# Kernel tuning notes

Measured on AMD Instinct MI355X. Metric: run time of the kernel, lower is better.

## Reference

```python
import jax, jax.numpy as jnp
import numpy as np

B, L, DIN, D, H, NL, NE, TOPK, DFF, NOUT = 128, 128, 6, 256, 8, 6, 8, 2, 1024, 5
NMOE = NL // 2
DK = D // H
EPS = 1e-5


def setup_inputs() -> dict:
    key = jax.random.key(0)
    ks = iter(jax.random.split(key, 32))
    s = 0.02
    rn = lambda shape, scale=s: jax.random.normal(next(ks), shape, dtype=jnp.float32) * scale
    return {
        "x": jax.random.normal(next(ks), (B, L, DIN), dtype=jnp.float32),
        "emb_w": rn((DIN, D)), "emb_b": jnp.zeros((D,), jnp.float32),
        # wave attention layers (stacked over NL)
        "wq": rn((NL, D, D)), "wk": rn((NL, D, D)), "wv": rn((NL, D, D)), "wo": rn((NL, D, D)),
        "wfreq": rn((NL, H), 0.1), "wphase": jnp.zeros((NL, H), jnp.float32),
        # MoE layers (stacked over NMOE, experts over NE)
        "rtw": rn((NMOE, D, NE)), "rtb": jnp.zeros((NMOE, NE), jnp.float32),
        "ew1": rn((NMOE, NE, D, DFF)), "eb1": jnp.zeros((NMOE, NE, DFF), jnp.float32),
        "ew2": rn((NMOE, NE, DFF, D)), "eb2": jnp.zeros((NMOE, NE, D), jnp.float32),
        "ln_g": jnp.ones((D,), jnp.float32), "ln_b": jnp.zeros((D,), jnp.float32),
        "pred_w": rn((D, NOUT)), "pred_b": jnp.zeros((NOUT,), jnp.float32),
        "unc_w": rn((D, NOUT)), "unc_b": jnp.zeros((NOUT,), jnp.float32),
    }


def _wave_attn(x, Wq, Wk, Wv, Wo, freq, phase):
    # x: (B, L, D)
    q = (x @ Wq).reshape(B, L, H, DK).transpose(0, 2, 1, 3)  # (B,H,L,DK)
    k = (x @ Wk).reshape(B, L, H, DK).transpose(0, 2, 1, 3)
    v = (x @ Wv).reshape(B, L, H, DK).transpose(0, 2, 1, 3)
    pos = jnp.arange(L, dtype=x.dtype)
    wave = jnp.cos(2.0 * np.pi * freq[:, None] * pos[None, :] + phase[:, None])  # (H,L)
    scores = jnp.einsum("bhqd,bhkd->bhqk", q, k) * (DK ** -0.5)
    scores = scores * wave[None, :, None, :]  # modulate along key axis
    attn = jax.nn.softmax(scores, axis=-1)
    out = jnp.einsum("bhqk,bhkd->bhqd", attn, v)
    out = out.transpose(0, 2, 1, 3).reshape(B, L, D)
    return out @ Wo


def _moe(x, rw, rb, w1, b1, w2, b2):
    # x: (B, L, D). Dense per-expert compute + top-k combine weights
    xf = x.reshape(-1, D)  # (T, D), T = B*L
    T = xf.shape[0]
    p = jax.nn.softmax(xf @ rw + rb, axis=-1)           # (T, NE)
    tw, ti = jax.lax.top_k(p, TOPK)                      # (T, TOPK)
    tw = tw / tw.sum(axis=-1, keepdims=True)
    comb = jnp.zeros((T, NE), xf.dtype).at[jnp.arange(T)[:, None], ti].add(tw)  # (T, NE)
    h = jax.nn.gelu(jnp.einsum("td,edf->etf", xf, w1) + b1[:, None, :], approximate=False)
    eo = jnp.einsum("etf,efd->etd", h, w2) + b2[:, None, :]  # (NE, T, D)
    out = jnp.einsum("te,etd->td", comb, eo)
    return out.reshape(B, L, D)


def _forward(x, emb_w, emb_b, wq, wk, wv, wo, wfreq, wphase,
             rtw, rtb, ew1, eb1, ew2, eb2, ln_g, ln_b,
             pred_w, pred_b, unc_w, unc_b):
    h = x @ emb_w + emb_b
    for i in range(NL):
        h = _wave_attn(h, wq[i], wk[i], wv[i], wo[i], wfreq[i], wphase[i]) + h
        if i % 2 == 0 and i // 2 < NMOE:
            m = i // 2
            h = _moe(h, rtw[m], rtb[m], ew1[m], eb1[m], ew2[m], eb2[m]) + h
    mu = h.mean(axis=-1, keepdims=True)
    var = ((h - mu) ** 2).mean(axis=-1, keepdims=True)
    h = (h - mu) * jax.lax.rsqrt(var + EPS) * ln_g + ln_b
    latent = h[:, -1, :]  # (B, D)
    pred = latent @ pred_w + pred_b
    uncertainty = jax.nn.softplus(latent @ unc_w + unc_b)
    return pred, uncertainty


def reference(x, emb_w, emb_b, wq, wk, wv, wo, wfreq, wphase,
              rtw, rtb, ew1, eb1, ew2, eb2, ln_g, ln_b,
              pred_w, pred_b, unc_w, unc_b):
    return _forward(x, emb_w, emb_b, wq, wk, wv, wo, wfreq, wphase,
                    rtw, rtb, ew1, eb1, ew2, eb2, ln_g, ln_b,
                    pred_w, pred_b, unc_w, unc_b)
```

## Files before the change

### kernel.cpp

```cpp
#include <hip/hip_runtime.h>
#include <hip/hip_bf16.h>
#include <math.h>

#define B_    128
#define L_    128
#define DIN   6
#define D_    256
#define H_    8
#define NL_   6
#define NE_   8
#define DFF_  1024
#define NOUT_ 5
#define T_    (B_*L_)
#define DK_   32
#define NDESC_MAX 136

typedef unsigned short u16;
typedef __hip_bfloat16 bf16;
typedef __attribute__((ext_vector_type(8))) short short8;
typedef __attribute__((ext_vector_type(8))) unsigned short ushort8v;
typedef __attribute__((ext_vector_type(4))) unsigned short ushort4v;
typedef __attribute__((ext_vector_type(4))) float floatx4;

__device__ const int S_PRE[16] = {
    0, 98304, 99840, 100096, 100144, 100192, 106336, 106360,
    130936, 137080, 137336, 137592, 138872, 138877, 140157, 140162};
__device__ const int S_SRC[15] = {0,1,2,7,8,9,10,12,14,15,16,17,18,19,20};
#define NSMALL 140162

struct SrcPtrs { const void* p[21]; };

__device__ __forceinline__ float bf2f(u16 u) {
    return __uint_as_float(((unsigned)u) << 16);
}
__device__ __forceinline__ u16 f2bf(float f) {
    union { bf16 b; u16 u; } c; c.b = __float2bfloat16(f); return c.u;
}
__device__ __forceinline__ float gelu_f(float x) {
    return 0.5f * x * (1.0f + erff(x * 0.70710678118654752f));
}

__device__ __forceinline__ void gl_lds16(const u16* g, u16* l) {
    __builtin_amdgcn_global_load_lds(
        (const __attribute__((address_space(1))) unsigned int*)g,
        (__attribute__((address_space(3))) unsigned int*)l,
        16, 0, 0);
}

__global__ __launch_bounds__(256)
void conv_small_kernel(SrcPtrs P, float* __restrict__ dst)
{
    const int i = blockIdx.x * 256 + threadIdx.x;
    if (i >= NSMALL) return;
    int seg = 0;
    #pragma unroll
    for (int s = 1; s < 15; ++s) seg += (i >= S_PRE[s]) ? 1 : 0;
    const int off = i - S_PRE[seg];
    const void* src = P.p[S_SRC[seg]];
    const bool isbf = (((const u16*)P.p[15])[0] == 0x3F80);
    if (isbf) dst[i] = bf2f(((const u16*)src)[off]);
    else      dst[i] = ((const float*)src)[off];
}

template<int KD, int ND>
__global__ __launch_bounds__(256)
void transpose_tiled(const void* __restrict__ src, const u16* __restrict__ probe,
                     u16* __restrict__ dst, long dzs, int noff)
{
    const int z  = blockIdx.x;
    const int k0 = blockIdx.y * 64;
    const int n0 = blockIdx.z * 64;
    __shared__ u16 tile[64][66];
    const int tid = threadIdx.x;
    const bool isbf = (probe[0] == 0x3F80);

    if (isbf) {
        const u16* s = (const u16*)src + (size_t)z * KD * ND + (size_t)k0 * ND + n0;
        #pragma unroll
        for (int p = 0; p < 2; ++p) {
            const int c  = p * 256 + tid;
            const int kk = c >> 3, nn = (c & 7) * 8;
            *(ushort8v*)&tile[kk][nn] = *(const ushort8v*)(s + (size_t)kk * ND + nn);
        }
    } else {
        const float* s = (const float*)src + (size_t)z * KD * ND + (size_t)k0 * ND + n0;
        #pragma unroll
        for (int p = 0; p < 2; ++p) {
            const int c  = p * 256 + tid;
            const int kk = c >> 3, nn = (c & 7) * 8;
            float4 v0 = *(const float4*)(s + (size_t)kk * ND + nn);
            float4 v1 = *(const float4*)(s + (size_t)kk * ND + nn + 4);
            ushort8v t;
            t[0]=f2bf(v0.x); t[1]=f2bf(v0.y); t[2]=f2bf(v0.z); t[3]=f2bf(v0.w);
            t[4]=f2bf(v1.x); t[5]=f2bf(v1.y); t[6]=f2bf(v1.z); t[7]=f2bf(v1.w);
            *(ushort8v*)&tile[kk][nn] = t;
        }
    }
    __syncthreads();

    u16* d = dst + (size_t)z * dzs + (size_t)(n0 + noff) * KD + k0;
    #pragma unroll
    for (int p = 0; p < 2; ++p) {
        const int c  = p * 256 + tid;
        const int nn = c >> 3, kk = (c & 7) * 8;
        ushort8v t;
        #pragma unroll
        for (int j = 0; j < 8; ++j) t[j] = tile[kk + j][nn];
        *(ushort8v*)&d[(size_t)nn * KD + kk] = t;
    }
}

__global__ __launch_bounds__(256)
void embed_kernel(const float* __restrict__ x, const float* __restrict__ emb_w,
                  const float* __restrict__ emb_b, float* __restrict__ h,
                  u16* __restrict__ hb)
{
    const int idx = blockIdx.x * 256 + threadIdx.x;
    const int t = idx >> 8;
    const int d = idx & 255;
    float acc = emb_b[d];
    #pragma unroll
    for (int j = 0; j < DIN; ++j)
        acc += x[t * DIN + j] * emb_w[j * D_ + d];
    h[idx]  = acc;
    hb[idx] = f2bf(acc);
}

template<int EPI, int MODE, int NT>
__global__ __launch_bounds__(512, 4)
void mfma_gemm(const u16* __restrict__ A, int lda,
               const u16* __restrict__ Wt, long wzs, int ldwt,
               const float* __restrict__ biasb, long bzs,
               void* __restrict__ CoutV, int ldc,
               u16* __restrict__ hbout, int Mfixed,
               const int* __restrict__ cnt, const int* __restrict__ base_,
               const int* __restrict__ atok,
               const int* __restrict__ de, const int* __restrict__ dr,
               const int* __restrict__ ndesc)
{
    int M, r0, sbase = 0, e = 0;
    if constexpr (MODE == 0) {
        M  = Mfixed;
        r0 = blockIdx.x * 256;
        if (r0 >= M) return;
    } else {
        const int i = blockIdx.x;
        if (i >= *ndesc) return;
        e     = de[i];
        r0    = dr[i] * 256;
        sbase = base_[e];
        M     = cnt[e];
    }
    const u16*   W    = Wt + (size_t)e * wzs;
    const float* bias = biasb ? (biasb + (size_t)e * bzs) : nullptr;
    const int col0 = blockIdx.y * 128;

    __shared__ __attribute__((aligned(16))) u16 As[2][256 * 32];
    __shared__ __attribute__((aligned(16))) u16 Bs[2][128 * 32];
    __shared__ int stok[256];

    const int tid  = threadIdx.x;
    const int lane = tid & 63;
    const int wave = tid >> 6;
    const int wm = wave & 3, wn = wave >> 2;

    if constexpr (MODE == 1) {
        if (tid < 256) {
            int rr = r0 + tid;
            if (rr >= M) rr = M - 1;
            stok[tid] = atok[sbase + rr];
        }
        __syncthreads();
    }

    const int ss  = (lane & 3) ^ ((lane >> 3) & 3);
    const int rA0 = wave * 16 + (lane >> 2);
    const int rA1 = rA0 + 128;
    const int rB  = tid >> 2;
    long ar0, ar1;
    if constexpr (MODE == 1) {
        ar0 = stok[rA0];
        ar1 = stok[rA1];
    } else {
        int rr0 = r0 + rA0; if (rr0 >= M) rr0 = M - 1;
        int rr1 = r0 + rA1; if (rr1 >= M) rr1 = M - 1;
        ar0 = (MODE == 2) ? (long)(sbase + rr0) : (long)rr0;
        ar1 = (MODE == 2) ? (long)(sbase + rr1) : (long)rr1;
    }
    const u16* ga0 = A + ar0 * (long)lda + ss * 8;
    const u16* ga1 = A + ar1 * (long)lda + ss * 8;
    const u16* gw0 = W + (size_t)(col0 + rB) * ldwt + ss * 8;

    floatx4 acc[4][4];
    #pragma unroll
    for (int i = 0; i < 4; ++i)
        #pragma unroll
        for (int j = 0; j < 4; ++j)
            acc[i][j] = (floatx4){0.f, 0.f, 0.f, 0.f};

    const int fm = wm * 64 + (lane & 15);
    const int fn = wn * 64 + (lane & 15);
    const int ps = (lane >> 4) ^ ((lane >> 1) & 3);

    auto STAGE = [&](int b, int kt) {
        const int ko = kt * 32;
        gl_lds16(ga0 + ko, &As[b][wave * 512 + lane * 8]);
        gl_lds16(ga1 + ko, &As[b][4096 + wave * 512 + lane * 8]);
        gl_lds16(gw0 + ko, &Bs[b][wave * 512 + lane * 8]);
    };

    STAGE(0, 0);
    __syncthreads();

    int buf = 0;
    for (int t = 0; t < NT; ++t) {
        if (t + 1 < NT) STAGE(buf ^ 1, t + 1);

        short8 af[4], bfr[4];
        #pragma unroll
        for (int i = 0; i < 4; ++i)
            af[i]  = *(const short8*)&As[buf][(fm + 16 * i) * 32 + ps * 8];
        #pragma unroll
        for (int j = 0; j < 4; ++j)
            bfr[j] = *(const short8*)&Bs[buf][(fn + 16 * j) * 32 + ps * 8];
        #pragma unroll
        for (int i = 0; i < 4; ++i)
            #pragma unroll
            for (int j = 0; j < 4; ++j)
                acc[i][j] = __builtin_amdgcn_mfma_f32_16x16x32_bf16(
                    af[i], bfr[j], acc[i][j], 0, 0, 0);

        __syncthreads();
        buf ^= 1;
    }

    const int er = wm * 64 + ((lane >> 4) << 2);
    const int ec = wn * 64 + (lane & 15);
    #pragma unroll
    for (int i = 0; i < 4; ++i) {
        #pragma unroll
        for (int reg = 0; reg < 4; ++reg) {
            const int lrow = r0 + er + i * 16 + reg;
            if (lrow >= M) continue;
            const long crow = (MODE == 0) ? (long)lrow : (long)(sbase + lrow);
            #pragma unroll
            for (int j = 0; j < 4; ++j) {
                const int cj = col0 + ec + j * 16;
                const float val = acc[i][j][reg];
                if constexpr (EPI == 0) {
                    ((u16*)CoutV)[crow * ldc + cj] = f2bf(val);
                } else if constexpr (EPI == 1) {
                    const size_t idx = crow * ldc + cj;
                    const float nv = ((float*)CoutV)[idx] + val;
                    ((float*)CoutV)[idx] = nv;
                    hbout[idx] = f2bf(nv);
                } else if constexpr (EPI == 2) {
                    ((u16*)CoutV)[crow * ldc + cj] = f2bf(gelu_f(val + bias[cj]));
                } else {
                    ((float*)CoutV)[crow * ldc + cj] = val + bias[cj];
                }
            }
        }
    }
}

__global__ __launch_bounds__(256)
void attn_kernel(const u16* __restrict__ qkv, u16* __restrict__ o,
                 const float* __restrict__ wfreq, const float* __restrict__ wphase)
{
    const int bh = blockIdx.x;
    const int b  = bh >> 3;
    const int hh = bh & 7;

    __shared__ __attribute__((aligned(16))) u16 Qs[128][40];
    __shared__ __attribute__((aligned(16))) u16 Ks[128][40];
    __shared__ __attribute__((aligned(16))) u16 Vt[32][136];
    __shared__ __attribute__((aligned(16))) u16 Ps[128][136];
    __shared__ float wavec[128];

    const int tid  = threadIdx.x;
    const int lane = tid & 63;
    const int w    = tid >> 6;
    const int col16 = lane & 15;
    const int quad  = lane >> 4;

    const long qbase = (long)b * L_ * 768 + hh * DK_;

    {
        const int row = tid >> 1;
        const int hf  = (tid & 1) * 16;
        const u16* src = qkv + qbase + (long)row * 768 + hf;
        *(ushort8v*)&Qs[row][hf]     = *(const ushort8v*)(src);
        *(ushort8v*)&Qs[row][hf + 8] = *(const ushort8v*)(src + 8);
        *(ushort8v*)&Ks[row][hf]     = *(const ushort8v*)(src + 256);
        *(ushort8v*)&Ks[row][hf + 8] = *(const ushort8v*)(src + 264);
        #pragma unroll
        for (int j = 0; j < 16; ++j)
            Vt[hf + j][row] = src[512 + j];
    }
    if (tid < L_) {
        float f2 = 6.2831853071795864769f * wfreq[hh];
        wavec[tid] = cosf(f2 * (float)tid + wphase[hh]);
    }
    __syncthreads();

    const float scale = 0.17677669529663687f;
    float wv8[8];
    #pragma unroll
    for (int ni = 0; ni < 8; ++ni)
        wv8[ni] = scale * wavec[ni * 16 + col16];

    const int m0 = w * 32;
    floatx4 accs[2][8];
    {
        short8 a0 = *(const short8*)&Qs[m0 + col16][quad * 8];
        short8 a1 = *(const short8*)&Qs[m0 + 16 + col16][quad * 8];
        #pragma unroll
        for (int ni = 0; ni < 8; ++ni) {
            short8 bf = *(const short8*)&Ks[ni * 16 + col16][quad * 8];
            accs[0][ni] = __builtin_amdgcn_mfma_f32_16x16x32_bf16(
                a0, bf, (floatx4){0.f,0.f,0.f,0.f}, 0, 0, 0);
            accs[1][ni] = __builtin_amdgcn_mfma_f32_16x16x32_bf16(
                a1, bf, (floatx4){0.f,0.f,0.f,0.f}, 0, 0, 0);
        }
    }
    #pragma unroll
    for (int mi = 0; mi < 2; ++mi)
        #pragma unroll
        for (int ni = 0; ni < 8; ++ni)
            #pragma unroll
            for (int reg = 0; reg < 4; ++reg)
                accs[mi][ni][reg] *= wv8[ni];

    #pragma unroll
    for (int mi = 0; mi < 2; ++mi) {
        #pragma unroll
        for (int reg = 0; reg < 4; ++reg) {
            float rmax = -1e30f;
            #pragma unroll
            for (int ni = 0; ni < 8; ++ni)
                rmax = fmaxf(rmax, accs[mi][ni][reg]);
            #pragma unroll
            for (int off = 1; off < 16; off <<= 1)
                rmax = fmaxf(rmax, __shfl_xor(rmax, off));
            float e[8], rsum = 0.0f;
            #pragma unroll
            for (int ni = 0; ni < 8; ++ni) {
                e[ni] = expf(accs[mi][ni][reg] - rmax);
                rsum += e[ni];
            }
            #pragma unroll
            for (int off = 1; off < 16; off <<= 1)
                rsum += __shfl_xor(rsum, off);
            const float inv = 1.0f / rsum;
            const int row = m0 + mi * 16 + quad * 4 + reg;
            #pragma unroll
            for (int ni = 0; ni < 8; ++ni)
                Ps[row][ni * 16 + col16] = f2bf(e[ni] * inv);
        }
    }
    __syncthreads();

    floatx4 acco[2][2];
    #pragma unroll
    for (int mi = 0; mi < 2; ++mi)
        #pragma unroll
        for (int nj = 0; nj < 2; ++nj)
            acco[mi][nj] = (floatx4){0.f,0.f,0.f,0.f};
    #pragma unroll
    for (int kk = 0; kk < 4; ++kk) {
        short8 a0 = *(const short8*)&Ps[m0 + col16][kk * 32 + quad * 8];
        short8 a1 = *(const short8*)&Ps[m0 + 16 + col16][kk * 32 + quad * 8];
        short8 b0 = *(const short8*)&Vt[col16][kk * 32 + quad * 8];
        short8 b1 = *(const short8*)&Vt[16 + col16][kk * 32 + quad * 8];
        acco[0][0] = __builtin_amdgcn_mfma_f32_16x16x32_bf16(a0, b0, acco[0][0], 0, 0, 0);
        acco[0][1] = __builtin_amdgcn_mfma_f32_16x16x32_bf16(a0, b1, acco[0][1], 0, 0, 0);
        acco[1][0] = __builtin_amdgcn_mfma_f32_16x16x32_bf16(a1, b0, acco[1][0], 0, 0, 0);
        acco[1][1] = __builtin_amdgcn_mfma_f32_16x16x32_bf16(a1, b1, acco[1][1], 0, 0, 0);
    }

    const long obase = (long)b * L_ * D_ + hh * DK_;
    #pragma unroll
    for (int mi = 0; mi < 2; ++mi)
        #pragma unroll
        for (int reg = 0; reg < 4; ++reg) {
            const int row = m0 + mi * 16 + quad * 4 + reg;
            #pragma unroll
            for (int nj = 0; nj < 2; ++nj)
                o[obase + (long)row * D_ + nj * 16 + col16] =
                    f2bf(acco[mi][nj][reg]);
        }
}

__global__ __launch_bounds__(256)
void router_kernel(const float* __restrict__ h, const float* __restrict__ rtw,
                   const float* __restrict__ rtb, int* __restrict__ te,
                   float* __restrict__ twt)
{
    const int tid  = threadIdx.x;
    const int lane = tid & 63;
    const int wv   = tid >> 6;
    const int t    = blockIdx.x * 4 + wv;

    const float4 hv = ((const float4*)(h + (long)t * D_))[lane];
    const float4* rp = (const float4*)rtw;

    float lg[NE_];
    #pragma unroll
    for (int e = 0; e < NE_; ++e) lg[e] = 0.0f;
    #pragma unroll
    for (int i = 0; i < 4; ++i) {
        const int d = lane * 4 + i;
        const float xv = (i == 0) ? hv.x : (i == 1) ? hv.y : (i == 2) ? hv.z : hv.w;
        float4 wa = rp[d * 2 + 0];
        float4 wb = rp[d * 2 + 1];
        lg[0] = fmaf(xv, wa.x, lg[0]);
        lg[1] = fmaf(xv, wa.y, lg[1]);
        lg[2] = fmaf(xv, wa.z, lg[2]);
        lg[3] = fmaf(xv, wa.w, lg[3]);
        lg[4] = fmaf(xv, wb.x, lg[4]);
        lg[5] = fmaf(xv, wb.y, lg[5]);
        lg[6] = fmaf(xv, wb.z, lg[6]);
        lg[7] = fmaf(xv, wb.w, lg[7]);
    }
    #pragma unroll
    for (int off = 1; off < 64; off <<= 1)
        #pragma unroll
        for (int e = 0; e < NE_; ++e)
            lg[e] += __shfl_xor(lg[e], off);

    if (lane == 0) {
        #pragma unroll
        for (int e = 0; e < NE_; ++e) lg[e] += rtb[e];
        int i1 = 0; float v1 = lg[0];
        #pragma unroll
        for (int e = 1; e < NE_; ++e) { if (lg[e] > v1) { v1 = lg[e]; i1 = e; } }
        int i2 = (i1 == 0) ? 1 : 0; float v2 = lg[i2];
        #pragma unroll
        for (int e = 0; e < NE_; ++e) {
            if (e != i1 && lg[e] > v2) { v2 = lg[e]; i2 = e; }
        }
        float r   = expf(v2 - v1);
        float wa1 = 1.0f / (1.0f + r);
        te[2 * t]     = i1;
        te[2 * t + 1] = i2;
        twt[2 * t]     = wa1;
        twt[2 * t + 1] = r * wa1;
    }
}

__global__ __launch_bounds__(512)
void countscan_kernel(const int* __restrict__ te, int* __restrict__ cnt,
                      int* __restrict__ base_, int* __restrict__ cursor,
                      int* __restrict__ de, int* __restrict__ dr,
                      int* __restrict__ ndesc)
{
    const int tid = threadIdx.x;
    int c[NE_];
    #pragma unroll
    for (int e = 0; e < NE_; ++e) c[e] = 0;
    for (int i = tid; i < 2 * T_; i += 512) {
        const int e = te[i];
        #pragma unroll
        for (int ee = 0; ee < NE_; ++ee) c[ee] += (e == ee) ? 1 : 0;
    }
    #pragma unroll
    for (int off = 1; off < 64; off <<= 1)
        #pragma unroll
        for (int e = 0; e < NE_; ++e)
            c[e] += __shfl_xor(c[e], off);

    __shared__ int wsum[8][NE_];
    const int lane = tid & 63, wv = tid >> 6;
    if (lane == 0)
        #pragma unroll
        for (int e = 0; e < NE_; ++e) wsum[wv][e] = c[e];
    __syncthreads();
    if (tid == 0) {
        int a = 0, n = 0;
        for (int e = 0; e < NE_; ++e) {
            int s = 0;
            for (int w = 0; w < 8; ++w) s += wsum[w][e];
            cnt[e] = s;
            base_[e] = a;
            a += s;
            const int nb = (s + 255) >> 8;
            for (int rb = 0; rb < nb; ++rb) {
                de[n] = e; dr[n] = rb; ++n;
            }
        }
        *ndesc = n;
    }
    if (tid < NE_) cursor[tid] = 0;
}

__global__ __launch_bounds__(256)
void scatter_kernel(const int* __restrict__ te, const int* __restrict__ base_,
                    int* __restrict__ cursor, int* __restrict__ atok,
                    int* __restrict__ tslot)
{
    __shared__ int lcnt[NE_];
    __shared__ int gb[NE_];
    const int tid = threadIdx.x;
    if (tid < NE_) lcnt[tid] = 0;
    __syncthreads();

    const int i0 = blockIdx.x * 512 + tid * 2;
    const int e0 = te[i0], e1 = te[i0 + 1];
    const int r0 = atomicAdd(&lcnt[e0], 1);
    const int r1 = atomicAdd(&lcnt[e1], 1);
    __syncthreads();
    if (tid < NE_) gb[tid] = atomicAdd(&cursor[tid], lcnt[tid]);
    __syncthreads();

    const int s0 = base_[e0] + gb[e0] + r0;
    const int s1 = base_[e1] + gb[e1] + r1;
    atok[s0] = i0 >> 1;
    atok[s1] = i0 >> 1;
    tslot[i0]     = s0;
    tslot[i0 + 1] = s1;
}

__global__ __launch_bounds__(256)
void combine_kernel(float* __restrict__ h, u16* __restrict__ hb,
                    const float* __restrict__ eo,
                    const float* __restrict__ twt, const int* __restrict__ tslot)
{
    const int i = blockIdx.x * 256 + threadIdx.x;
    const int t = i >> 6;
    const int g = i & 63;
    const int s0 = tslot[2 * t], s1 = tslot[2 * t + 1];
    const float w0 = twt[2 * t], w1 = twt[2 * t + 1];
    float4 a  = ((const float4*)(eo + (size_t)s0 * D_))[g];
    float4 b  = ((const float4*)(eo + (size_t)s1 * D_))[g];
    float4 hv = ((const float4*)(h + (size_t)t * D_))[g];
    hv.x += w0 * a.x + w1 * b.x;
    hv.y += w0 * a.y + w1 * b.y;
    hv.z += w0 * a.z + w1 * b.z;
    hv.w += w0 * a.w + w1 * b.w;
    ((float4*)(h + (size_t)t * D_))[g] = hv;
    ushort4v pk;
    pk[0] = f2bf(hv.x); pk[1] = f2bf(hv.y); pk[2] = f2bf(hv.z); pk[3] = f2bf(hv.w);
    *(ushort4v*)&hb[(size_t)t * D_ + g * 4] = pk;
}

__global__ __launch_bounds__(256)
void final_kernel(const float* __restrict__ h, const float* __restrict__ ln_g,
                  const float* __restrict__ ln_b, const float* __restrict__ pred_w,
                  const float* __restrict__ pred_b, const float* __restrict__ unc_w,
                  const float* __restrict__ unc_b, float* __restrict__ out)
{
    const int b = blockIdx.x;
    const int d = threadIdx.x;
    const long t = (long)b * L_ + (L_ - 1);
    const float val = h[t * D_ + d];

    __shared__ float red[4];
    __shared__ float lat[D_];

    float s = val;
    #pragma unroll
    for (int off = 32; off > 0; off >>= 1) s += __shfl_down(s, off);
    if ((d & 63) == 0) red[d >> 6] = s;
    __syncthreads();
    const float mean = (red[0] + red[1] + red[2] + red[3]) * (1.0f / D_);
    __syncthreads();

    const float dv = val - mean;
    s = dv * dv;
    #pragma unroll
    for (int off = 32; off > 0; off >>= 1) s += __shfl_down(s, off);
    if ((d & 63) == 0) red[d >> 6] = s;
    __syncthreads();
    const float var = (red[0] + red[1] + red[2] + red[3]) * (1.0f / D_);

    lat[d] = dv * rsqrtf(var + 1e-5f) * ln_g[d] + ln_b[d];
    __syncthreads();

    if (d < 2 * NOUT_) {
        const int j = d % NOUT_;
        const int sel = d / NOUT_;
        const float* w  = sel ? unc_w : pred_w;
        const float* bb = sel ? unc_b : pred_b;
        float acc = bb[j];
        for (int dd = 0; dd < D_; ++dd)
            acc = fmaf(lat[dd], w[dd * NOUT_ + j], acc);
        if (sel) acc = log1pf(expf(acc));
        out[sel * (B_ * NOUT_) + b * NOUT_ + j] = acc;
    }
}

extern "C" void kernel_launch(void* const* d_in, const int* in_sizes, int n_in,
                              void* d_out, int out_size, void* d_ws, size_t ws_size,
                              hipStream_t stream)
{
    (void)in_sizes; (void)n_in; (void)out_size; (void)ws_size;

    char* ws = (char*)d_ws;
    size_t off = 0;
    auto alloc = [&](size_t bytes) {
        size_t cur = off;
        off += (bytes + 255) & ~(size_t)255;
        return (void*)(ws + cur);
    };
    float* cs     = (float*)alloc((size_t)NSMALL * 4);
    u16*   qkvt   = (u16*)  alloc((size_t)NL_ * 768 * 256 * 2);
    u16*   wot    = (u16*)  alloc((size_t)NL_ * 256 * 256 * 2);
    u16*   ew1t   = (u16*)  alloc((size_t)3 * NE_ * DFF_ * D_ * 2);
    u16*   ew2t   = (u16*)  alloc((size_t)3 * NE_ * D_ * DFF_ * 2);
    float* h      = (float*)alloc((size_t)T_ * D_ * 4);
    u16*   hb     = (u16*)  alloc((size_t)T_ * D_ * 2);
    char*  uni    = (char*) alloc((size_t)2 * T_ * DFF_ * 2 + (size_t)2 * T_ * D_ * 4);
    u16*   qkvb   = (u16*)  uni;
    u16*   ob     = (u16*)  (uni + (size_t)T_ * 768 * 2 + 256);
    u16*   hidden = (u16*)  uni;
    float* eo     = (float*)(uni + (size_t)2 * T_ * DFF_ * 2);
    int*   te     = (int*)  alloc((size_t)2 * T_ * 4);
    float* twt    = (float*)alloc((size_t)2 * T_ * 4);
    int*   atok   = (int*)  alloc((size_t)2 * T_ * 4);
    int*   tslot  = (int*)  alloc((size_t)2 * T_ * 4);
    int*   cnt    = (int*)  alloc(64 * 4);
    int*   base_  = (int*)  alloc(64 * 4);
    int*   cursor = (int*)  alloc(64 * 4);
    int*   de     = (int*)  alloc(NDESC_MAX * 4);
    int*   dr     = (int*)  alloc(NDESC_MAX * 4);
    int*   ndesc  = (int*)  alloc(64 * 4);

    SrcPtrs P;
    for (int i = 0; i < 21; ++i) P.p[i] = d_in[i];
    const u16* probe = (const u16*)d_in[15];

    conv_small_kernel<<<(NSMALL + 255) / 256, 256, 0, stream>>>(P, cs);
    transpose_tiled<256,256><<<dim3(NL_, 4, 4), 256, 0, stream>>>(
        d_in[3], probe, qkvt, 768L * 256, 0);
    transpose_tiled<256,256><<<dim3(NL_, 4, 4), 256, 0, stream>>>(
        d_in[4], probe, qkvt, 768L * 256, 256);
    transpose_tiled<256,256><<<dim3(NL_, 4, 4), 256, 0, stream>>>(
        d_in[5], probe, qkvt, 768L * 256, 512);
    transpose_tiled<256,256><<<dim3(NL_, 4, 4), 256, 0, stream>>>(
        d_in[6], probe, wot, 65536L, 0);
    transpose_tiled<256,1024><<<dim3(24, 4, 16), 256, 0, stream>>>(
        d_in[11], probe, ew1t, 262144L, 0);
    transpose_tiled<1024,256><<<dim3(24, 16, 4), 256, 0, stream>>>(
        d_in[13], probe, ew2t, 262144L, 0);

    const float* x      = cs;
    const float* emb_w  = cs + 98304;
    const float* emb_b  = cs + 99840;
    const float* wfreq  = cs + 100096;
    const float* wphase = cs + 100144;
    const float* rtw    = cs + 100192;
    const float* rtb    = cs + 106336;
    const float* eb1    = cs + 106360;
    const float* eb2    = cs + 130936;
    const float* ln_g   = cs + 137080;
    const float* ln_b   = cs + 137336;
    const float* pred_w = cs + 137592;
    const float* pred_b = cs + 138872;
    const float* unc_w  = cs + 138877;
    const float* unc_b  = cs + 140157;

    embed_kernel<<<(T_ * D_) / 256, 256, 0, stream>>>(x, emb_w, emb_b, h, hb);

    for (int i = 0; i < NL_; ++i) {
        mfma_gemm<0, 0, 8><<<dim3(T_/256, 6, 1), 512, 0, stream>>>(
            hb, D_, qkvt + (size_t)i * 768 * 256, 0, 256,
            nullptr, 0, qkvb, 768, nullptr, T_,
            nullptr, nullptr, nullptr, nullptr, nullptr, nullptr);
        attn_kernel<<<B_ * H_, 256, 0, stream>>>(qkvb, ob,
                                                 wfreq + i * H_, wphase + i * H_);
        mfma_gemm<1, 0, 8><<<dim3(T_/256, 2, 1), 512, 0, stream>>>(
            ob, D_, wot + (size_t)i * 65536, 0, 256,
            nullptr, 0, h, D_, hb, T_,
            nullptr, nullptr, nullptr, nullptr, nullptr, nullptr);

        if (i % 2 == 0) {
            const int m = i / 2;
            const u16* w1t = ew1t + (size_t)m * NE_ * DFF_ * D_;
            const u16* w2t = ew2t + (size_t)m * NE_ * D_ * DFF_;
            const float* b1 = eb1 + (size_t)m * NE_ * DFF_;
            const float* b2 = eb2 + (size_t)m * NE_ * D_;
            router_kernel<<<T_ / 4, 256, 0, stream>>>(
                h, rtw + (size_t)m * D_ * NE_, rtb + m * NE_, te, twt);
            countscan_kernel<<<1, 512, 0, stream>>>(te, cnt, base_, cursor,
                                                    de, dr, ndesc);
            scatter_kernel<<<(2 * T_) / 512, 256, 0, stream>>>(te, base_, cursor,
                                                               atok, tslot);
            mfma_gemm<2, 1, 8><<<dim3(NDESC_MAX, DFF_/128, 1), 512, 0, stream>>>(
                hb, D_, w1t, (long)DFF_ * D_, 256,
                b1, DFF_, hidden, DFF_, nullptr, 0,
                cnt, base_, atok, de, dr, ndesc);
            mfma_gemm<3, 2, 32><<<dim3(NDESC_MAX, D_/128, 1), 512, 0, stream>>>(
                hidden, DFF_, w2t, (long)D_ * DFF_, DFF_,
                b2, D_, eo, D_, nullptr, 0,
                cnt, base_, nullptr, de, dr, ndesc);
            combine_kernel<<<(T_ * 64) / 256, 256, 0, stream>>>(h, hb, eo,
                                                                twt, tslot);
        }
    }

    final_kernel<<<B_, 256, 0, stream>>>(h, ln_g, ln_b, pred_w, pred_b,
                                         unc_w, unc_b, (float*)d_out);
}
```

Before: 952.9 us.

## Replace LDS-staged GEMM with direct global fragment loads and smaller 128-row tiles

The MFMA GEMM no longer stages A and W tiles through double-buffered shared memory via global_load_lds. Each wave now loads its bf16 fragments straight from global memory, with no barriers, and relies on caches for reuse. The tile shrinks from 256x128 with 512 threads to 128x128 with 256 threads, and the MoE descriptor granularity, grid sizes and NDESC_MAX are adjusted to match. The aim is to remove barrier and LDS overhead and to improve load balance across the variable-size expert groups. The cost is that each element is re-read from global or L2 by several waves without sharing, which raises memory traffic.

```diff
diff --git a/kernel.cpp b/kernel.cpp
--- a/kernel.cpp
+++ b/kernel.cpp
@@ -13,7 +13,7 @@
 #define NOUT_ 5
 #define T_    (B_*L_)
 #define DK_   32
-#define NDESC_MAX 136
+#define NDESC_MAX 264
 
 typedef unsigned short u16;
 typedef __hip_bfloat16 bf16;
@@ -38,13 +38,6 @@
 }
 __device__ __forceinline__ float gelu_f(float x) {
     return 0.5f * x * (1.0f + erff(x * 0.70710678118654752f));
-}
-
-__device__ __forceinline__ void gl_lds16(const u16* g, u16* l) {
-    __builtin_amdgcn_global_load_lds(
-        (const __attribute__((address_space(1))) unsigned int*)g,
-        (__attribute__((address_space(3))) unsigned int*)l,
-        16, 0, 0);
 }
 
 __global__ __launch_bounds__(256)
@@ -127,7 +120,7 @@
 }
 
 template<int EPI, int MODE, int NT>
-__global__ __launch_bounds__(512, 4)
+__global__ __launch_bounds__(256)
 void mfma_gemm(const u16* __restrict__ A, int lda,
                const u16* __restrict__ Wt, long wzs, int ldwt,
                const float* __restrict__ biasb, long bzs,
@@ -141,13 +134,13 @@
     int M, r0, sbase = 0, e = 0;
     if constexpr (MODE == 0) {
         M  = Mfixed;
-        r0 = blockIdx.x * 256;
+        r0 = blockIdx.x * 128;
         if (r0 >= M) return;
     } else {
         const int i = blockIdx.x;
         if (i >= *ndesc) return;
         e     = de[i];
-        r0    = dr[i] * 256;
+        r0    = dr[i] * 128;
         sbase = base_[e];
         M     = cnt[e];
     }
@@ -155,41 +148,30 @@
     const float* bias = biasb ? (biasb + (size_t)e * bzs) : nullptr;
     const int col0 = blockIdx.y * 128;
 
-    __shared__ __attribute__((aligned(16))) u16 As[2][256 * 32];
-    __shared__ __attribute__((aligned(16))) u16 Bs[2][128 * 32];
-    __shared__ int stok[256];
-
     const int tid  = threadIdx.x;
     const int lane = tid & 63;
     const int wave = tid >> 6;
-    const int wm = wave & 3, wn = wave >> 2;
-
-    if constexpr (MODE == 1) {
-        if (tid < 256) {
-            int rr = r0 + tid;
-            if (rr >= M) rr = M - 1;
-            stok[tid] = atok[sbase + rr];
-        }
-        __syncthreads();
-    }
-
-    const int ss  = (lane & 3) ^ ((lane >> 3) & 3);
-    const int rA0 = wave * 16 + (lane >> 2);
-    const int rA1 = rA0 + 128;
-    const int rB  = tid >> 2;
-    long ar0, ar1;
-    if constexpr (MODE == 1) {
-        ar0 = stok[rA0];
-        ar1 = stok[rA1];
-    } else {
-        int rr0 = r0 + rA0; if (rr0 >= M) rr0 = M - 1;
-        int rr1 = r0 + rA1; if (rr1 >= M) rr1 = M - 1;
-        ar0 = (MODE == 2) ? (long)(sbase + rr0) : (long)rr0;
-        ar1 = (MODE == 2) ? (long)(sbase + rr1) : (long)rr1;
-    }
-    const u16* ga0 = A + ar0 * (long)lda + ss * 8;
-    const u16* ga1 = A + ar1 * (long)lda + ss * 8;
-    const u16* gw0 = W + (size_t)(col0 + rB) * ldwt + ss * 8;
+    const int wm = wave & 1, wn = wave >> 1;
+
+    const int fm = wm * 64 + (lane & 15);
+    const int fn = wn * 64 + (lane & 15);
+    const int fk = (lane >> 4) * 8;
+
+    const u16* pa[4];
+    const u16* pb[4];
+    #pragma unroll
+    for (int i = 0; i < 4; ++i) {
+        int rr = r0 + fm + 16 * i;
+        if (rr >= M) rr = M - 1;
+        long arow;
+        if constexpr (MODE == 1)      arow = atok[sbase + rr];
+        else if constexpr (MODE == 2) arow = (long)(sbase + rr);
+        else                          arow = (long)rr;
+        pa[i] = A + arow * (long)lda + fk;
+    }
+    #pragma unroll
+    for (int j = 0; j < 4; ++j)
+        pb[j] = W + (size_t)(col0 + fn + 16 * j) * ldwt + fk;
 
     floatx4 acc[4][4];
     #pragma unroll
@@ -198,40 +180,20 @@
         for (int j = 0; j < 4; ++j)
             acc[i][j] = (floatx4){0.f, 0.f, 0.f, 0.f};
 
-    const int fm = wm * 64 + (lane & 15);
-    const int fn = wn * 64 + (lane & 15);
-    const int ps = (lane >> 4) ^ ((lane >> 1) & 3);
-
-    auto STAGE = [&](int b, int kt) {
-        const int ko = kt * 32;
-        gl_lds16(ga0 + ko, &As[b][wave * 512 + lane * 8]);
-        gl_lds16(ga1 + ko, &As[b][4096 + wave * 512 + lane * 8]);
-        gl_lds16(gw0 + ko, &Bs[b][wave * 512 + lane * 8]);
-    };
-
-    STAGE(0, 0);
-    __syncthreads();
-
-    int buf = 0;
+    #pragma unroll 4
     for (int t = 0; t < NT; ++t) {
-        if (t + 1 < NT) STAGE(buf ^ 1, t + 1);
-
+        const int ko = t * 32;
         short8 af[4], bfr[4];
         #pragma unroll
-        for (int i = 0; i < 4; ++i)
-            af[i]  = *(const short8*)&As[buf][(fm + 16 * i) * 32 + ps * 8];
-        #pragma unroll
-        for (int j = 0; j < 4; ++j)
-            bfr[j] = *(const short8*)&Bs[buf][(fn + 16 * j) * 32 + ps * 8];
+        for (int i = 0; i < 4; ++i) af[i]  = *(const short8*)(pa[i] + ko);
+        #pragma unroll
+        for (int j = 0; j < 4; ++j) bfr[j] = *(const short8*)(pb[j] + ko);
         #pragma unroll
         for (int i = 0; i < 4; ++i)
             #pragma unroll
             for (int j = 0; j < 4; ++j)
                 acc[i][j] = __builtin_amdgcn_mfma_f32_16x16x32_bf16(
                     af[i], bfr[j], acc[i][j], 0, 0, 0);
-
-        __syncthreads();
-        buf ^= 1;
     }
 
     const int er = wm * 64 + ((lane >> 4) << 2);
@@ -484,7 +446,7 @@
             cnt[e] = s;
             base_[e] = a;
             a += s;
-            const int nb = (s + 255) >> 8;
+            const int nb = (s + 127) >> 7;
             for (int rb = 0; rb < nb; ++rb) {
                 de[n] = e; dr[n] = rb; ++n;
             }
@@ -663,13 +625,13 @@
     embed_kernel<<<(T_ * D_) / 256, 256, 0, stream>>>(x, emb_w, emb_b, h, hb);
 
     for (int i = 0; i < NL_; ++i) {
-        mfma_gemm<0, 0, 8><<<dim3(T_/256, 6, 1), 512, 0, stream>>>(
+        mfma_gemm<0, 0, 8><<<dim3(T_/128, 6, 1), 256, 0, stream>>>(
             hb, D_, qkvt + (size_t)i * 768 * 256, 0, 256,
             nullptr, 0, qkvb, 768, nullptr, T_,
             nullptr, nullptr, nullptr, nullptr, nullptr, nullptr);
         attn_kernel<<<B_ * H_, 256, 0, stream>>>(qkvb, ob,
                                                  wfreq + i * H_, wphase + i * H_);
-        mfma_gemm<1, 0, 8><<<dim3(T_/256, 2, 1), 512, 0, stream>>>(
+        mfma_gemm<1, 0, 8><<<dim3(T_/128, 2, 1), 256, 0, stream>>>(
             ob, D_, wot + (size_t)i * 65536, 0, 256,
             nullptr, 0, h, D_, hb, T_,
             nullptr, nullptr, nullptr, nullptr, nullptr, nullptr);
@@ -686,11 +648,11 @@
                                                     de, dr, ndesc);
             scatter_kernel<<<(2 * T_) / 512, 256, 0, stream>>>(te, base_, cursor,
                                                                atok, tslot);
-            mfma_gemm<2, 1, 8><<<dim3(NDESC_MAX, DFF_/128, 1), 512, 0, stream>>>(
+            mfma_gemm<2, 1, 8><<<dim3(NDESC_MAX, DFF_/128, 1), 256, 0, stream>>>(
                 hb, D_, w1t, (long)DFF_ * D_, 256,
                 b1, DFF_, hidden, DFF_, nullptr, 0,
                 cnt, base_, atok, de, dr, ndesc);
-            mfma_gemm<3, 2, 32><<<dim3(NDESC_MAX, D_/128, 1), 512, 0, stream>>>(
+            mfma_gemm<3, 2, 32><<<dim3(NDESC_MAX, D_/128, 1), 256, 0, stream>>>(
                 hidden, DFF_, w2t, (long)D_ * DFF_, DFF_,
                 b2, D_, eo, D_, nullptr, 0,
                 cnt, base_, nullptr, de, dr, ndesc);
```

New measurement: 1.455 ms. 52.7% more time.
